# Performance work log

Measured on AMD Instinct MI355X. Metric: run time of the kernel, lower is better.

## Reference

```python
import jax, jax.numpy as jnp
import numpy as np

N = 100_000      # nodes
E = 800_000      # edges (avg degree 8)
D_IN = 16        # embedding_dimension
H = 128          # hidden_dimension
OUT = 3          # out_dim
NEG_SLOPE = 0.01 # LeakyReLU default


def setup_inputs() -> dict:
    key = jax.random.key(0)
    ks = jax.random.split(key, 9)
    s = 0.05
    return {
        "feature": jax.random.normal(ks[0], (N, D_IN), jnp.float32),
        "edge_index": jax.random.randint(ks[1], (2, E), 0, N, dtype=jnp.int64),
        "edge_type": jax.random.randint(ks[2], (E,), 0, 2, dtype=jnp.int64),
        "W_in": jax.random.normal(ks[3], (D_IN, H), jnp.float32) * s,
        "b_in": jnp.zeros((H,), jnp.float32),
        "W1": jax.random.normal(ks[4], (H, H), jnp.float32) * s,
        "b1": jnp.zeros((H,), jnp.float32),
        "W2": jax.random.normal(ks[5], (H, H), jnp.float32) * s,
        "b2": jnp.zeros((H,), jnp.float32),
        "W_out": jax.random.normal(ks[6], (H, OUT), jnp.float32) * s,
        "b_out": jnp.zeros((OUT,), jnp.float32),
    }


def gcn_conv(x, W, b, src, dst, n):
    """PyG GCNConv: linear -> add self-loops -> D^-1/2 A D^-1/2 aggregation -> bias."""
    h = x @ W                                   # [N, H]
    loop = jnp.arange(n, dtype=src.dtype)
    src_sl = jnp.concatenate([src, loop])       # [E+N]
    dst_sl = jnp.concatenate([dst, loop])
    deg = jax.ops.segment_sum(jnp.ones_like(dst_sl, dtype=h.dtype), dst_sl, num_segments=n)
    dinv = jax.lax.rsqrt(jnp.maximum(deg, 1.0))  # deg >= 1 due to self-loops
    norm = dinv[src_sl] * dinv[dst_sl]          # [E+N]
    msg = h[src_sl] * norm[:, None]             # gather + scale, [E+N, H]
    out = jax.ops.segment_sum(msg, dst_sl, num_segments=n)  # scatter-add
    return out + b


def reference(feature, edge_index, edge_type, W_in, b_in, W1, b1, W2, b2, W_out, b_out):
    # edge_type is accepted but unused, exactly as in the torch forward.
    x = jax.nn.leaky_relu(feature.astype(jnp.float32) @ W_in + b_in, NEG_SLOPE)
    src, dst = edge_index[0], edge_index[1]
    x = gcn_conv(x, W1, b1, src, dst, N)
    # F.dropout with training=False is identity (inference path)
    x = gcn_conv(x, W2, b2, src, dst, N)
    return x @ W_out + b_out
```

## Files before the change

kernel.cpp:

```cpp
#include <hip/hip_runtime.h>
#include <hip/hip_bf16.h>
#include <cstdint>

#define DIN 16
#define HD  128
#define RNG 2048
#define LB  11
#define MAXB 64
#define PB  256

static __device__ __forceinline__ void fma4(float4& a, float s, const float4 v) {
    a.x = fmaf(s, v.x, a.x);
    a.y = fmaf(s, v.y, a.y);
    a.z = fmaf(s, v.z, a.z);
    a.w = fmaf(s, v.w, a.w);
}
static __device__ __forceinline__ void add4(float4& a, const float4 v) {
    a.x += v.x; a.y += v.y; a.z += v.z; a.w += v.w;
}

__global__ __launch_bounds__(256) void k_histfold(const int* __restrict__ dst,
                                                  int* __restrict__ hist,
                                                  int E, int R, int CHK,
                                                  const float* __restrict__ W1,
                                                  const float* __restrict__ b1,
                                                  const float* __restrict__ W2,
                                                  const float* __restrict__ b2,
                                                  const float* __restrict__ Wout,
                                                  const float* __restrict__ bout,
                                                  float* __restrict__ Wcp,
                                                  float* __restrict__ cbuf) {
    int tid = threadIdx.x;
    if (blockIdx.x < PB) {
        __shared__ int h[MAXB];
        for (int i = tid; i < R; i += 256) h[i] = 0;
        __syncthreads();
        int e0 = blockIdx.x * CHK;
        int e1 = e0 + CHK; if (e1 > E) e1 = E;
        for (int e = e0 + tid; e < e1; e += 256) atomicAdd(&h[dst[e] >> LB], 1);
        __syncthreads();
        for (int i = tid; i < R; i += 256) hist[i * PB + blockIdx.x] = h[i];
        return;
    }
    __shared__ float sT[HD * 3];
    for (int idx = tid; idx < HD * 3; idx += 256) {
        int k = idx / 3, o = idx - 3 * k;
        float s = 0.f;
        for (int j = 0; j < HD; j++) s = fmaf(W2[k * HD + j], Wout[j * 3 + o], s);
        sT[idx] = s;
    }
    if (tid < 3) {
        float s = bout[tid];
        for (int j = 0; j < HD; j++) s = fmaf(b2[j], Wout[j * 3 + tid], s);
        cbuf[3 + tid] = s;
    }
    __syncthreads();
    if (tid < 3) {
        float s = 0.f;
        for (int j = 0; j < HD; j++) s = fmaf(b1[j], sT[j * 3 + tid], s);
        cbuf[tid] = s;
    }
    for (int idx = tid; idx < HD * 3; idx += 256) {
        int k = idx / 3, o = idx - 3 * k;
        float s = 0.f;
        for (int j = 0; j < HD; j++) s = fmaf(W1[k * HD + j], sT[j * 3 + o], s);
        Wcp[k * 4 + o] = s;
    }
    for (int idx = tid; idx < HD; idx += 256) Wcp[idx * 4 + 3] = 0.f;
}

__global__ __launch_bounds__(1024) void k_scanmlp(int* __restrict__ hist, int nh,
                                                  const float* __restrict__ F,
                                                  const float* __restrict__ Win,
                                                  const float* __restrict__ bin,
                                                  const float4* __restrict__ Wcp,
                                                  float4* __restrict__ Y, int N) {
    int tid = threadIdx.x;
    if (blockIdx.x == 0) {
        __shared__ int sd[1024];
        int CH = (nh + 1023) / 1024;
        int c0 = tid * CH;
        int c1 = c0 + CH; if (c1 > nh) c1 = nh;
        int sum = 0;
        for (int i = c0; i < c1; i++) sum += hist[i];
        sd[tid] = sum;
        __syncthreads();
        for (int off = 1; off < 1024; off <<= 1) {
            int t = (tid >= off) ? sd[tid - off] : 0;
            __syncthreads();
            sd[tid] += t;
            __syncthreads();
        }
        int base = sd[tid] - sum;
        for (int i = c0; i < c1; i++) { int t = hist[i]; hist[i] = base; base += t; }
        return;
    }
    __shared__ float4 sWinT[DIN * HD / 4];
    __shared__ float4 sWcT[HD];
    __shared__ float4 sBin[HD / 4];
    __shared__ float  sF[64 * DIN];
    if (tid < DIN * HD / 4) {
        int k = tid >> 5, rem = tid & 31, l = rem >> 1, c = rem & 1;
        sWinT[k * 32 + c * 16 + l] = ((const float4*)Win)[tid];
    } else if (tid < DIN * HD / 4 + HD) {
        int i = tid - DIN * HD / 4;
        sWcT[(i & 7) * 16 + (i >> 3)] = Wcp[i];
    } else if (tid < DIN * HD / 4 + HD + HD / 4) {
        int i = tid - DIN * HD / 4 - HD;
        sBin[i] = ((const float4*)bin)[i];
    }
    int base = (blockIdx.x - 1) * 64;
    {
        int node = base + (tid >> 4);
        sF[tid] = (node < N) ? F[(size_t)base * DIN + tid] : 0.f;
    }
    __syncthreads();
    int l = tid & 15;
    int g = tid >> 4;
    int node = base + g;
    if (node >= N) return;
    float4 h0 = sBin[l * 2 + 0];
    float4 h1 = sBin[l * 2 + 1];
    #pragma unroll
    for (int k = 0; k < DIN; k++) {
        float f = sF[g * DIN + k];
        fma4(h0, f, sWinT[k * 32 + l]);
        fma4(h1, f, sWinT[k * 32 + 16 + l]);
    }
    h0.x = h0.x > 0.f ? h0.x : 0.01f * h0.x;
    h0.y = h0.y > 0.f ? h0.y : 0.01f * h0.y;
    h0.z = h0.z > 0.f ? h0.z : 0.01f * h0.z;
    h0.w = h0.w > 0.f ? h0.w : 0.01f * h0.w;
    h1.x = h1.x > 0.f ? h1.x : 0.01f * h1.x;
    h1.y = h1.y > 0.f ? h1.y : 0.01f * h1.y;
    h1.z = h1.z > 0.f ? h1.z : 0.01f * h1.z;
    h1.w = h1.w > 0.f ? h1.w : 0.01f * h1.w;
    float hv[8] = {h0.x, h0.y, h0.z, h0.w, h1.x, h1.y, h1.z, h1.w};
    float a0 = 0.f, a1 = 0.f, a2 = 0.f;
    #pragma unroll
    for (int jj = 0; jj < 8; jj++) {
        float4 wc = sWcT[jj * 16 + l];
        a0 = fmaf(hv[jj], wc.x, a0);
        a1 = fmaf(hv[jj], wc.y, a1);
        a2 = fmaf(hv[jj], wc.z, a2);
    }
    #pragma unroll
    for (int off = 8; off > 0; off >>= 1) {
        a0 += __shfl_down(a0, off, 16);
        a1 += __shfl_down(a1, off, 16);
        a2 += __shfl_down(a2, off, 16);
    }
    if (l == 0) Y[node] = make_float4(a0, a1, a2, 1.0f);
}

__global__ __launch_bounds__(256) void k_part(const int* __restrict__ src,
                                              const int* __restrict__ dst,
                                              const int* __restrict__ off,
                                              int2* __restrict__ ebin,
                                              int E, int R, int CHK) {
    __shared__ int cur[MAXB];
    int tid = threadIdx.x;
    int b = blockIdx.x;
    for (int i = tid; i < R; i += 256) cur[i] = off[i * PB + b];
    __syncthreads();
    int e0 = b * CHK;
    int e1 = e0 + CHK; if (e1 > E) e1 = E;
    for (int e = e0 + tid; e < e1; e += 256) {
        int s = src[e], d = dst[e];
        int pos = atomicAdd(&cur[d >> LB], 1);
        ebin[pos] = make_int2(s, d & (RNG - 1));
    }
}

__global__ __launch_bounds__(1024) void k_csr(const int2* __restrict__ ebin,
                                              const int* __restrict__ off,
                                              const float4* __restrict__ Y,
                                              int* __restrict__ rowptr,
                                              int* __restrict__ ecsr,
                                              float* __restrict__ dinv,
                                              float4* __restrict__ Ys,
                                              int N, int E, int R) {
    __shared__ int c[RNG];
    __shared__ int sd[1024];
    int tid = threadIdx.x;
    int b = blockIdx.x;
    c[tid] = 0; c[tid + 1024] = 0;
    __syncthreads();
    int e0 = off[b * PB];
    int e1 = (b + 1 < R) ? off[(b + 1) * PB] : E;
    for (int e = e0 + tid; e < e1; e += 1024) atomicAdd(&c[ebin[e].y], 1);
    __syncthreads();
    int v0 = c[2 * tid], v1 = c[2 * tid + 1];
    int ts = v0 + v1;
    sd[tid] = ts;
    __syncthreads();
    for (int o = 1; o < 1024; o <<= 1) {
        int t = (tid >= o) ? sd[tid - o] : 0;
        __syncthreads();
        sd[tid] += t;
        __syncthreads();
    }
    int rp0 = e0 + sd[tid] - ts;
    int rp1 = rp0 + v0;
    int n0 = b * RNG + 2 * tid;
    if (n0 <= N) rowptr[n0] = rp0;
    if (n0 + 1 <= N) rowptr[n0 + 1] = rp1;
    if (b == R - 1 && tid == 1023) rowptr[N] = E;
    if (n0 < N) {
        float di = rsqrtf((float)v0 + 1.0f);
        dinv[n0] = di;
        float4 y = Y[n0];
        Ys[n0] = make_float4(di * y.x, di * y.y, di * y.z, di);
    }
    if (n0 + 1 < N) {
        float di = rsqrtf((float)v1 + 1.0f);
        dinv[n0 + 1] = di;
        float4 y = Y[n0 + 1];
        Ys[n0 + 1] = make_float4(di * y.x, di * y.y, di * y.z, di);
    }
    c[2 * tid] = rp0;
    c[2 * tid + 1] = rp1;
    __syncthreads();
    for (int e = e0 + tid; e < e1; e += 1024) {
        int2 ed = ebin[e];
        int pos = atomicAdd(&c[ed.y], 1);
        ecsr[pos] = ed.x;
    }
}

__global__ __launch_bounds__(256) void k_aggA(const int* __restrict__ rowptr,
                                              const int* __restrict__ ecsr,
                                              const float4* __restrict__ Ys,
                                              const float* __restrict__ dinv,
                                              float4* __restrict__ Z1s, int N) {
    int n = blockIdx.x * blockDim.x + threadIdx.x;
    if (n >= N) return;
    int beg = rowptr[n], end = rowptr[n + 1];
    float4 acc = Ys[n];
    int j = beg;
    for (; j + 4 <= end; j += 4) {
        int s0 = ecsr[j], s1 = ecsr[j + 1], s2 = ecsr[j + 2], s3 = ecsr[j + 3];
        float4 a = Ys[s0], b = Ys[s1], c = Ys[s2], d = Ys[s3];
        add4(acc, a); add4(acc, b); add4(acc, c); add4(acc, d);
    }
    for (; j < end; j++) add4(acc, Ys[ecsr[j]]);
    float di = dinv[n];
    float d2 = di * di;
    Z1s[n] = make_float4(d2 * acc.x, d2 * acc.y, d2 * acc.z, d2 * acc.w);
}

__global__ __launch_bounds__(256) void k_aggB(const int* __restrict__ rowptr,
                                              const int* __restrict__ ecsr,
                                              const float4* __restrict__ Z1s,
                                              const float* __restrict__ dinv,
                                              const float* __restrict__ cbuf,
                                              float* __restrict__ out, int N) {
    int n = blockIdx.x * blockDim.x + threadIdx.x;
    if (n >= N) return;
    int beg = rowptr[n], end = rowptr[n + 1];
    float4 acc = Z1s[n];
    float di = dinv[n];
    float r = acc.w / di;
    int j = beg;
    for (; j + 4 <= end; j += 4) {
        int s0 = ecsr[j], s1 = ecsr[j + 1], s2 = ecsr[j + 2], s3 = ecsr[j + 3];
        float4 a = Z1s[s0], b = Z1s[s1], c = Z1s[s2], d = Z1s[s3];
        add4(acc, a); add4(acc, b); add4(acc, c); add4(acc, d);
    }
    for (; j < end; j++) add4(acc, Z1s[ecsr[j]]);
    out[(size_t)n * 3 + 0] = di * acc.x + r * cbuf[0] + cbuf[3];
    out[(size_t)n * 3 + 1] = di * acc.y + r * cbuf[1] + cbuf[4];
    out[(size_t)n * 3 + 2] = di * acc.z + r * cbuf[2] + cbuf[5];
}

extern "C" void kernel_launch(void* const* d_in, const int* in_sizes, int n_in,
                              void* d_out, int out_size, void* d_ws, size_t ws_size,
                              hipStream_t stream) {
    const float* feat = (const float*)d_in[0];
    const int*   ei   = (const int*)d_in[1];
    const float* Win  = (const float*)d_in[3];
    const float* bin  = (const float*)d_in[4];
    const float* W1   = (const float*)d_in[5];
    const float* b1   = (const float*)d_in[6];
    const float* W2   = (const float*)d_in[7];
    const float* b2   = (const float*)d_in[8];
    const float* Wout = (const float*)d_in[9];
    const float* bout = (const float*)d_in[10];
    float* out = (float*)d_out;

    int N = in_sizes[0] / DIN;
    int E = in_sizes[2];
    const int* src = ei;
    const int* dst = ei + E;

    int R = (N + RNG - 1) >> LB;
    int CHK = (E + PB - 1) / PB;
    int NH = R * PB;
    int XB = (N + 63) / 64;

    char* p = (char*)d_ws;
    auto alloc = [&](size_t bytes) -> char* {
        char* q = p;
        p += (bytes + 511) & ~(size_t)511;
        return q;
    };
    int*    hist   = (int*)alloc((size_t)NH * 4);
    int2*   ebin   = (int2*)alloc((size_t)E * 8);
    int*    ecsr   = (int*)alloc((size_t)E * 4);
    int*    rowptr = (int*)alloc((size_t)(N + 1) * 4);
    float4* Y      = (float4*)alloc((size_t)N * 16);
    float4* Ys     = (float4*)alloc((size_t)N * 16);
    float4* Z1s    = (float4*)alloc((size_t)N * 16);
    float*  dinv   = (float*)alloc((size_t)N * 4);
    float*  Wcp    = (float*)alloc(HD * 4 * 4);
    float*  cbuf   = (float*)alloc(8 * 4);

    k_histfold<<<PB + 1, 256, 0, stream>>>(dst, hist, E, R, CHK,
                                           W1, b1, W2, b2, Wout, bout, Wcp, cbuf);
    k_scanmlp<<<1 + XB, 1024, 0, stream>>>(hist, NH, feat, Win, bin,
                                           (const float4*)Wcp, Y, N);
    k_part<<<PB, 256, 0, stream>>>(src, dst, hist, ebin, E, R, CHK);
    k_csr<<<R, 1024, 0, stream>>>(ebin, hist, Y, rowptr, ecsr, dinv, Ys, N, E, R);
    k_aggA<<<(N + 255) / 256, 256, 0, stream>>>(rowptr, ecsr, Ys, dinv, Z1s, N);
    k_aggB<<<(N + 255) / 256, 256, 0, stream>>>(rowptr, ecsr, Z1s, dinv, cbuf, out, N);
}
```

Baseline: 160.2 us.

## Pack edge bins into 32-bit words, use a shuffle scan, and batch neighbor gathers

Each binned edge is now stored as one 32-bit word (source shifted left plus the local destination bits) instead of an int2. This halves the partition and CSR-build traffic. The block-wide Hillis-Steele scan in the CSR builder is replaced by a two-level wavefront shuffle scan, which removes many barriers. Both aggregation kernels now issue 12 neighbor gathers unconditionally from vector-loaded indices, padded with zeros at the end of the CSR array, and mask the adds by degree. This buys more loads in flight at the cost of extra gathers for low-degree nodes and possibly unaligned 16-byte index loads.

```diff
diff --git a/kernel.cpp b/kernel.cpp
--- a/kernel.cpp
+++ b/kernel.cpp
@@ -156,7 +156,7 @@
 __global__ __launch_bounds__(256) void k_part(const int* __restrict__ src,
                                               const int* __restrict__ dst,
                                               const int* __restrict__ off,
-                                              int2* __restrict__ ebin,
+                                              int* __restrict__ ebin,
                                               int E, int R, int CHK) {
     __shared__ int cur[MAXB];
     int tid = threadIdx.x;
@@ -168,11 +168,11 @@
     for (int e = e0 + tid; e < e1; e += 256) {
         int s = src[e], d = dst[e];
         int pos = atomicAdd(&cur[d >> LB], 1);
-        ebin[pos] = make_int2(s, d & (RNG - 1));
-    }
-}
-
-__global__ __launch_bounds__(1024) void k_csr(const int2* __restrict__ ebin,
+        ebin[pos] = (s << LB) | (d & (RNG - 1));
+    }
+}
+
+__global__ __launch_bounds__(1024) void k_csr(const int* __restrict__ ebin,
                                               const int* __restrict__ off,
                                               const float4* __restrict__ Y,
                                               int* __restrict__ rowptr,
@@ -181,26 +181,39 @@
                                               float4* __restrict__ Ys,
                                               int N, int E, int R) {
     __shared__ int c[RNG];
-    __shared__ int sd[1024];
+    __shared__ int swv[16];
     int tid = threadIdx.x;
     int b = blockIdx.x;
     c[tid] = 0; c[tid + 1024] = 0;
     __syncthreads();
     int e0 = off[b * PB];
     int e1 = (b + 1 < R) ? off[(b + 1) * PB] : E;
-    for (int e = e0 + tid; e < e1; e += 1024) atomicAdd(&c[ebin[e].y], 1);
+    for (int e = e0 + tid; e < e1; e += 1024) atomicAdd(&c[ebin[e] & (RNG - 1)], 1);
     __syncthreads();
     int v0 = c[2 * tid], v1 = c[2 * tid + 1];
     int ts = v0 + v1;
-    sd[tid] = ts;
-    __syncthreads();
-    for (int o = 1; o < 1024; o <<= 1) {
-        int t = (tid >= o) ? sd[tid - o] : 0;
-        __syncthreads();
-        sd[tid] += t;
-        __syncthreads();
-    }
-    int rp0 = e0 + sd[tid] - ts;
+    int lane = tid & 63, wid = tid >> 6;
+    int sc = ts;
+    #pragma unroll
+    for (int o = 1; o < 64; o <<= 1) {
+        int t = __shfl_up(sc, o, 64);
+        if (lane >= o) sc += t;
+    }
+    if (lane == 63) swv[wid] = sc;
+    __syncthreads();
+    if (tid < 16) {
+        int v = swv[tid];
+        int s2 = v;
+        #pragma unroll
+        for (int o = 1; o < 16; o <<= 1) {
+            int t = __shfl_up(s2, o, 16);
+            if (tid >= o) s2 += t;
+        }
+        swv[tid] = s2 - v;
+    }
+    __syncthreads();
+    int excl = sc - ts + swv[wid];
+    int rp0 = e0 + excl;
     int rp1 = rp0 + v0;
     int n0 = b * RNG + 2 * tid;
     if (n0 <= N) rowptr[n0] = rp0;
@@ -222,10 +235,11 @@
     c[2 * tid + 1] = rp1;
     __syncthreads();
     for (int e = e0 + tid; e < e1; e += 1024) {
-        int2 ed = ebin[e];
-        int pos = atomicAdd(&c[ed.y], 1);
-        ecsr[pos] = ed.x;
-    }
+        int ed = ebin[e];
+        int pos = atomicAdd(&c[ed & (RNG - 1)], 1);
+        ecsr[pos] = ed >> LB;
+    }
+    if (b == 0 && tid < 16) ecsr[E + tid] = 0;
 }
 
 __global__ __launch_bounds__(256) void k_aggA(const int* __restrict__ rowptr,
@@ -236,14 +250,19 @@
     int n = blockIdx.x * blockDim.x + threadIdx.x;
     if (n >= N) return;
     int beg = rowptr[n], end = rowptr[n + 1];
+    int deg = end - beg;
     float4 acc = Ys[n];
-    int j = beg;
-    for (; j + 4 <= end; j += 4) {
-        int s0 = ecsr[j], s1 = ecsr[j + 1], s2 = ecsr[j + 2], s3 = ecsr[j + 3];
-        float4 a = Ys[s0], b = Ys[s1], c = Ys[s2], d = Ys[s3];
-        add4(acc, a); add4(acc, b); add4(acc, c); add4(acc, d);
-    }
-    for (; j < end; j++) add4(acc, Ys[ecsr[j]]);
+    int4 q0 = *(const int4*)(ecsr + beg);
+    int4 q1 = *(const int4*)(ecsr + beg + 4);
+    int4 q2 = *(const int4*)(ecsr + beg + 8);
+    int si[12] = {q0.x, q0.y, q0.z, q0.w, q1.x, q1.y, q1.z, q1.w,
+                  q2.x, q2.y, q2.z, q2.w};
+    float4 g[12];
+    #pragma unroll
+    for (int k = 0; k < 12; k++) g[k] = Ys[si[k]];
+    #pragma unroll
+    for (int k = 0; k < 12; k++) if (k < deg) add4(acc, g[k]);
+    for (int j = beg + 12; j < end; j++) add4(acc, Ys[ecsr[j]]);
     float di = dinv[n];
     float d2 = di * di;
     Z1s[n] = make_float4(d2 * acc.x, d2 * acc.y, d2 * acc.z, d2 * acc.w);
@@ -258,16 +277,21 @@
     int n = blockIdx.x * blockDim.x + threadIdx.x;
     if (n >= N) return;
     int beg = rowptr[n], end = rowptr[n + 1];
+    int deg = end - beg;
     float4 acc = Z1s[n];
     float di = dinv[n];
     float r = acc.w / di;
-    int j = beg;
-    for (; j + 4 <= end; j += 4) {
-        int s0 = ecsr[j], s1 = ecsr[j + 1], s2 = ecsr[j + 2], s3 = ecsr[j + 3];
-        float4 a = Z1s[s0], b = Z1s[s1], c = Z1s[s2], d = Z1s[s3];
-        add4(acc, a); add4(acc, b); add4(acc, c); add4(acc, d);
-    }
-    for (; j < end; j++) add4(acc, Z1s[ecsr[j]]);
+    int4 q0 = *(const int4*)(ecsr + beg);
+    int4 q1 = *(const int4*)(ecsr + beg + 4);
+    int4 q2 = *(const int4*)(ecsr + beg + 8);
+    int si[12] = {q0.x, q0.y, q0.z, q0.w, q1.x, q1.y, q1.z, q1.w,
+                  q2.x, q2.y, q2.z, q2.w};
+    float4 g[12];
+    #pragma unroll
+    for (int k = 0; k < 12; k++) g[k] = Z1s[si[k]];
+    #pragma unroll
+    for (int k = 0; k < 12; k++) if (k < deg) add4(acc, g[k]);
+    for (int j = beg + 12; j < end; j++) add4(acc, Z1s[ecsr[j]]);
     out[(size_t)n * 3 + 0] = di * acc.x + r * cbuf[0] + cbuf[3];
     out[(size_t)n * 3 + 1] = di * acc.y + r * cbuf[1] + cbuf[4];
     out[(size_t)n * 3 + 2] = di * acc.z + r * cbuf[2] + cbuf[5];
@@ -305,8 +329,8 @@
         return q;
     };
     int*    hist   = (int*)alloc((size_t)NH * 4);
-    int2*   ebin   = (int2*)alloc((size_t)E * 8);
-    int*    ecsr   = (int*)alloc((size_t)E * 4);
+    int*    ebin   = (int*)alloc((size_t)E * 4);
+    int*    ecsr   = (int*)alloc(((size_t)E + 16) * 4);
     int*    rowptr = (int*)alloc((size_t)(N + 1) * 4);
     float4* Y      = (float4*)alloc((size_t)N * 16);
     float4* Ys     = (float4*)alloc((size_t)N * 16);
```

After: 160.7 us. No clear change (+0.3%).
